# Optimization experiments

Hardware: AMD Instinct MI355X
Metric: run time of the kernel (lower is better)

The kernel has to match this reference:

```python
import jax, jax.numpy as jnp
import numpy as np

# Param packing order: [capacitance_x, capacitance_y] + for each direction in
# (ax, by, xy, yx, xx, yy): [conductance, mean, std, pot]  -> total 26 scalars.
_DIR = {"ax": 0, "by": 1, "xy": 2, "yx": 3, "xx": 4, "yy": 5}

B, T = 4096, 4096


def setup_inputs() -> dict:
    key = jax.random.key(0)
    inputs = jax.random.normal(key, (B, T, 2), dtype=jnp.float32)
    # initializer constants from the keras layer
    params = jnp.asarray([1.0, 1.0] + [0.001, 0.3, 3.0, 1.0] * 6, dtype=jnp.float32)
    return {"inputs": inputs, "params": params}


def reference(inputs, params):
    cap_x, cap_y = params[0], params[1]

    def syn(d, pre, post):
        i = 2 + 4 * _DIR[d]
        g, mean, std, pot = params[i], params[i + 1], params[i + 2], params[i + 3]
        return g * jax.nn.sigmoid(std * (pre - mean)) * (pot - post)

    def step(state, inp):
        x, y = state                      # each [B, 1]
        a, b = inp[:, :1], inp[:, 1:]     # each [B, 1]
        cur_x = syn("ax", a, x) + syn("yx", y, x) + syn("xx", x, x)
        cur_y = syn("by", b, y) + syn("xy", x, y) + syn("yy", y, y)
        x = x + cur_x / cap_x
        y = y + cur_y / cap_y
        out = jnp.concatenate((x, y), axis=-1)  # [B, 2]
        return (x, y), out

    bsz = inputs.shape[0]
    x0 = jnp.zeros((bsz, 1), inputs.dtype)
    y0 = jnp.ones((bsz, 1), inputs.dtype)   # initial state = concat(zeros, ones)
    _, outs = jax.lax.scan(step, (x0, y0), jnp.swapaxes(inputs, 0, 1))  # [T, B, 2]
    return jnp.swapaxes(outs, 0, 1)  # [B, T, 2]
```

## Files before the change

### kernel.cpp

```cpp
#include <hip/hip_runtime.h>

#define TLEN  4096
#define NROWS 4096
#define RPB   32
#define K     32
#define NC    (TLEN / K)
#define LDPAD 66
#define SGSL  (16 * 32)
#define STSL  (RPB * LDPAD)
#define UN    8

__device__ __forceinline__ float fexp2(float x) { return __builtin_amdgcn_exp2f(x); }
__device__ __forceinline__ float frcp(float x)  { return __builtin_amdgcn_rcpf(x); }
__device__ __forceinline__ float sigz(float z)  { return frcp(1.0f + fexp2(z)); }

__device__ __forceinline__ float lane_swap1(float v) {
    int r = __builtin_amdgcn_update_dpp(0, __float_as_int(v), 0xB1, 0xF, 0xF, true);
    return __int_as_float(r);
}

__device__ void run_fast(const float* __restrict__ inp, const float* __restrict__ prm,
                         float* __restrict__ out,
                         float4* __restrict__ sgbuf,
                         float*  __restrict__ st) {
    const int tid  = threadIdx.x;
    const int wid  = tid >> 6;
    const int lane = tid & 63;
    const int R0   = blockIdx.x * RPB;
    const float L2E = 1.4426950408889634f;
    float2* __restrict__ out2 = (float2*)out;

    if (wid == 1) {
        const int r = lane & 31, h = lane >> 5;
        const float c1x = -prm[4] * L2E, c0x = prm[4] * prm[3] * L2E;
        const float c1y = -prm[8] * L2E, c0y = prm[8] * prm[7] * L2E;
        const float4* __restrict__ src = (const float4*)inp + (size_t)(R0 + r) * (TLEN / 2);

        auto produce = [&](int c) {
            float4* sl = sgbuf + ((c & 1) ? SGSL : 0);
            const int base = c * 16 + h * 8;
#pragma unroll
            for (int j = 0; j < 8; ++j) {
                float4 v = src[base + j];
                float4 o;
                o.x = sigz(__builtin_fmaf(c1x, v.x, c0x));
                o.y = sigz(__builtin_fmaf(c1y, v.y, c0y));
                o.z = sigz(__builtin_fmaf(c1x, v.z, c0x));
                o.w = sigz(__builtin_fmaf(c1y, v.w, c0y));
                sl[(h * 8 + j) * 32 + r] = o;
            }
        };
        auto flush = [&](int c) {
            const float* sl = st + ((c & 1) ? STSL : 0);
            const int col = lane & 31;
#pragma unroll
            for (int j = 0; j < 16; ++j) {
                int ro = 2 * j + (lane >> 5);
                float2 v = *(const float2*)&sl[ro * LDPAD + col * 2];
                out2[(size_t)(R0 + ro) * TLEN + (size_t)c * K + col] = v;
            }
        };

        produce(0);
        __syncthreads();
        for (int c = 0; c < NC; ++c) {
            if (c + 1 < NC) produce(c + 1);
            if (c >= 1)     flush(c - 1);
            __syncthreads();
        }
        flush(NC - 1);
    } else {
        const int r_  = lane >> 1;
        const int par = lane & 1;
        const int inB = par ? 6 : 2, sfB = par ? 22 : 18, t2B = par ? 10 : 14;
        const float ic  = 1.0f / prm[par];
        const float g1  = prm[sfB] * ic, P1 = g1 * prm[sfB + 3], Gn1 = -g1;
        const float g2  = prm[t2B] * ic, P2 = g2 * prm[t2B + 3], Gn2 = -g2;
        const float gA  = prm[inB] * ic, PA = gA * prm[inB + 3], GnA = -gA;
        const float sdz = prm[sfB + 2];
        const float c1s = -sdz * L2E, c0s = sdz * prm[sfB + 1] * L2E;

        float x   = par ? 1.0f : 0.0f;
        float sig = sigz(__builtin_fmaf(c1s, x, c0s));
        float u   = __builtin_fmaf(-sig, sig, sig);
        float q   = 0.5f - sig;

        auto step = [&](float sg, float* wp, int t) {
            float Av  = __builtin_fmaf(GnA, x, PA);
            float t1v = __builtin_fmaf(Gn1, x, P1);
            float t2v = __builtin_fmaf(Gn2, x, P2);
            float m   = sg * Av;
            float b2  = __builtin_fmaf(sig, t1v, m);
            float sc  = lane_swap1(sig);
            float dx  = __builtin_fmaf(sc, t2v, b2);
            x = x + dx;
            wp[2 * t] = x;
            float dz = sdz * dx;
            float tt = __builtin_fmaf(q, dz, 1.0f);
            float aa = dz * tt;
            sig = __builtin_fmaf(u, aa, sig);
            u   = __builtin_fmaf(-sig, sig, sig);
            q   = 0.5f - sig;
        };

        __syncthreads();
        for (int c = 0; c < NC; ++c) {
            const float4* lb = sgbuf + ((c & 1) ? SGSL : 0);
            float* wp = st + ((c & 1) ? STSL : 0) + r_ * LDPAD + par;
            float4 f0 = lb[r_];
            float4 f1 = lb[32 + r_];
#pragma unroll
            for (int tp = 0; tp < 16; ++tp) {
                float4 f = f0; f0 = f1;
                if (tp < 14) f1 = lb[(tp + 2) * 32 + r_];
                step(par ? f.y : f.x, wp, 2 * tp);
                step(par ? f.w : f.z, wp, 2 * tp + 1);
            }
            sig = sigz(__builtin_fmaf(c1s, x, c0s));
            u   = __builtin_fmaf(-sig, sig, sig);
            q   = 0.5f - sig;
            __syncthreads();
        }
    }
}

struct LaneConst {
    float c1_in, c0_in, c1_sf, c0_sf, c1_ot, c0_ot;
    float gS_in, gS_cr, gS_sf, gP_in, gP_cr, gP_sf;
};

template<bool SHARED>
__device__ __forceinline__ float do_step_exact(float s, float pre_in, const LaneConst& k) {
    float sig_in = sigz(__builtin_fmaf(k.c1_in, pre_in, k.c0_in));
    float sig_sf = sigz(__builtin_fmaf(k.c1_sf, s, k.c0_sf));
    float sig_ot;
    if (SHARED) sig_ot = sig_sf;
    else        sig_ot = sigz(__builtin_fmaf(k.c1_ot, s, k.c0_ot));
    float sig_cr = lane_swap1(sig_ot);
    float S = __builtin_fmaf(k.gS_in, sig_in, __builtin_fmaf(k.gS_cr, sig_cr, k.gS_sf * sig_sf));
    float P = __builtin_fmaf(k.gP_in, sig_in, __builtin_fmaf(k.gP_cr, sig_cr, k.gP_sf * sig_sf));
    return s + __builtin_fmaf(S, -s, P);
}

template<bool SHARED>
__device__ void run_exact(const float* __restrict__ inp, const float* __restrict__ prm,
                          float* __restrict__ out) {
    const int tid = blockIdx.x * 128 + threadIdx.x;
    const int row = tid >> 1;
    if (row >= NROWS) return;
    const int par = tid & 1;
    const float L2E = 1.4426950408889634f;
    const int inB = par ? 6 : 2, sfB = par ? 22 : 18, otB = par ? 14 : 10, crB = par ? 10 : 14;
    const float invc = 1.0f / prm[par];
    LaneConst k;
    float sd = prm[inB + 2], mn = prm[inB + 1];
    k.c1_in = -sd * L2E; k.c0_in = sd * mn * L2E;
    sd = prm[sfB + 2]; mn = prm[sfB + 1];
    k.c1_sf = -sd * L2E; k.c0_sf = sd * mn * L2E;
    sd = prm[otB + 2]; mn = prm[otB + 1];
    k.c1_ot = -sd * L2E; k.c0_ot = sd * mn * L2E;
    k.gS_in = prm[inB] * invc; k.gP_in = k.gS_in * prm[inB + 3];
    k.gS_sf = prm[sfB] * invc; k.gP_sf = k.gS_sf * prm[sfB + 3];
    k.gS_cr = prm[crB] * invc; k.gP_cr = k.gS_cr * prm[crB + 3];

    const float4* __restrict__ src = (const float4*)inp + (size_t)row * (TLEN / 2);
    float* __restrict__ dst = out + (size_t)row * (TLEN * 2) + par;
    float s = par ? 1.0f : 0.0f;

    float4 cur[UN], nxt[UN];
#pragma unroll
    for (int j = 0; j < UN; ++j) cur[j] = src[j];
    const int NIT = TLEN / (2 * UN);
    for (int it = 0; it < NIT; ++it) {
        if (it + 1 < NIT) {
#pragma unroll
            for (int j = 0; j < UN; ++j) nxt[j] = src[(it + 1) * UN + j];
        }
        float* dptr = dst + it * (UN * 4);
#pragma unroll
        for (int j = 0; j < UN; ++j) {
            float4 f = cur[j];
            s = do_step_exact<SHARED>(s, par ? f.y : f.x, k);
            dptr[j * 4] = s;
            s = do_step_exact<SHARED>(s, par ? f.w : f.z, k);
            dptr[j * 4 + 2] = s;
        }
#pragma unroll
        for (int j = 0; j < UN; ++j) cur[j] = nxt[j];
    }
}

__global__ __launch_bounds__(128, 1)
void memcell_scan(const float* __restrict__ inp, const float* __restrict__ prm,
                  float* __restrict__ out) {
    __shared__ float4 sgbuf[2 * SGSL];
    __shared__ float  st[2 * STSL];

    const bool shared = (prm[11] == prm[19]) && (prm[12] == prm[20]) &&
                        (prm[15] == prm[23]) && (prm[16] == prm[24]);
    const float capx = prm[0], capy = prm[1];
    const bool gpos = prm[2] >= 0.f && prm[6] >= 0.f && prm[10] >= 0.f &&
                      prm[14] >= 0.f && prm[18] >= 0.f && prm[22] >= 0.f &&
                      capx > 0.f && capy > 0.f;
    const float sx = (prm[2] + prm[14] + prm[18]) / capx;
    const float sy = (prm[6] + prm[10] + prm[22]) / capy;
    const float lox = fminf(0.f, fminf(prm[5], fminf(prm[17], prm[21])));
    const float hix = fmaxf(0.f, fmaxf(prm[5], fmaxf(prm[17], prm[21])));
    const float loy = fminf(1.f, fminf(prm[9], fminf(prm[13], prm[25])));
    const float hiy = fmaxf(1.f, fmaxf(prm[9], fmaxf(prm[13], prm[25])));
    const float wbx = prm[20] * sx * (hix - lox), wby = prm[24] * sy * (hiy - loy);
    const float zmx = prm[20] * fmaxf(fabsf(lox - prm[19]), fabsf(hix - prm[19]));
    const float zmy = prm[24] * fmaxf(fabsf(loy - prm[23]), fabsf(hiy - prm[23]));
    const bool fast = shared && gpos && sx <= 0.25f && sy <= 0.25f &&
                      wbx <= 0.05f && wby <= 0.05f && zmx <= 20.f && zmy <= 20.f;
    if (fast) {
        run_fast(inp, prm, out, sgbuf, st);
    } else {
        if (shared) run_exact<true >(inp, prm, out);
        else        run_exact<false>(inp, prm, out);
    }
}

extern "C" void kernel_launch(void* const* d_in, const int* in_sizes, int n_in,
                              void* d_out, int out_size, void* d_ws, size_t ws_size,
                              hipStream_t stream) {
    (void)in_sizes; (void)n_in; (void)d_ws; (void)ws_size; (void)out_size;
    const float* inp = (const float*)d_in[0];
    const float* prm = (const float*)d_in[1];
    float* out = (float*)d_out;
    memcell_scan<<<dim3(NROWS / RPB), dim3(128), 0, stream>>>(inp, prm, out);
}
```

Baseline: 351.3 us.

## Precompute input-synapse coefficients in producer and compute exact sigmoid per step

The producer wave now folds the input-synapse conductance and potential into the staged values, so the consumer's input term becomes a single FMA per step. The consumer replaces the Taylor-style incremental sigmoid update with an exact exp2/rcp sigmoid on every step. This removes the parameter-range guard that selected the fast path. Shared-memory layouts are reworked so each lane (one row and one state variable) reads its own float4 and writes its own padded row. The change puts a transcendental back on the serial dependency chain in exchange for accuracy and a simpler input term, and it doubles the staged LDS footprint.

```diff
diff --git a/kernel.cpp b/kernel.cpp
--- a/kernel.cpp
+++ b/kernel.cpp
@@ -5,9 +5,9 @@
 #define RPB   32
 #define K     32
 #define NC    (TLEN / K)
-#define LDPAD 66
-#define SGSL  (16 * 32)
-#define STSL  (RPB * LDPAD)
+#define SGSL  (16 * 64)
+#define STP   33
+#define STSL  (64 * STP)
 #define UN    8
 
 __device__ __forceinline__ float fexp2(float x) { return __builtin_amdgcn_exp2f(x); }
@@ -34,20 +34,27 @@
         const int r = lane & 31, h = lane >> 5;
         const float c1x = -prm[4] * L2E, c0x = prm[4] * prm[3] * L2E;
         const float c1y = -prm[8] * L2E, c0y = prm[8] * prm[7] * L2E;
+        const float gAx = prm[2] / prm[0], PAx = gAx * prm[5], GnAx = -gAx;
+        const float gAy = prm[6] / prm[1], PAy = gAy * prm[9], GnAy = -gAy;
         const float4* __restrict__ src = (const float4*)inp + (size_t)(R0 + r) * (TLEN / 2);
 
         auto produce = [&](int c) {
             float4* sl = sgbuf + ((c & 1) ? SGSL : 0);
-            const int base = c * 16 + h * 8;
+            const int base = c * 16;
 #pragma unroll
             for (int j = 0; j < 8; ++j) {
-                float4 v = src[base + j];
-                float4 o;
-                o.x = sigz(__builtin_fmaf(c1x, v.x, c0x));
-                o.y = sigz(__builtin_fmaf(c1y, v.y, c0y));
-                o.z = sigz(__builtin_fmaf(c1x, v.z, c0x));
-                o.w = sigz(__builtin_fmaf(c1y, v.w, c0y));
-                sl[(h * 8 + j) * 32 + r] = o;
+                const int tp = h * 8 + j;
+                float4 v = src[base + tp];
+                float sx0 = sigz(__builtin_fmaf(c1x, v.x, c0x));
+                float sy0 = sigz(__builtin_fmaf(c1y, v.y, c0y));
+                float sx1 = sigz(__builtin_fmaf(c1x, v.z, c0x));
+                float sy1 = sigz(__builtin_fmaf(c1y, v.w, c0y));
+                float4 ox; ox.x = GnAx * sx0; ox.y = PAx * sx0;
+                           ox.z = GnAx * sx1; ox.w = PAx * sx1;
+                float4 oy; oy.x = GnAy * sy0; oy.y = PAy * sy0;
+                           oy.z = GnAy * sy1; oy.w = PAy * sy1;
+                sl[tp * 64 + 2 * r]     = ox;
+                sl[tp * 64 + 2 * r + 1] = oy;
             }
         };
         auto flush = [&](int c) {
@@ -56,7 +63,9 @@
 #pragma unroll
             for (int j = 0; j < 16; ++j) {
                 int ro = 2 * j + (lane >> 5);
-                float2 v = *(const float2*)&sl[ro * LDPAD + col * 2];
+                float2 v;
+                v.x = sl[(2 * ro)     * STP + col];
+                v.y = sl[(2 * ro + 1) * STP + col];
                 out2[(size_t)(R0 + ro) * TLEN + (size_t)c * K + col] = v;
             }
         };
@@ -70,55 +79,42 @@
         }
         flush(NC - 1);
     } else {
-        const int r_  = lane >> 1;
         const int par = lane & 1;
-        const int inB = par ? 6 : 2, sfB = par ? 22 : 18, t2B = par ? 10 : 14;
+        const int sfB = par ? 22 : 18, t2B = par ? 10 : 14;
         const float ic  = 1.0f / prm[par];
         const float g1  = prm[sfB] * ic, P1 = g1 * prm[sfB + 3], Gn1 = -g1;
         const float g2  = prm[t2B] * ic, P2 = g2 * prm[t2B + 3], Gn2 = -g2;
-        const float gA  = prm[inB] * ic, PA = gA * prm[inB + 3], GnA = -gA;
         const float sdz = prm[sfB + 2];
         const float c1s = -sdz * L2E, c0s = sdz * prm[sfB + 1] * L2E;
 
         float x   = par ? 1.0f : 0.0f;
         float sig = sigz(__builtin_fmaf(c1s, x, c0s));
-        float u   = __builtin_fmaf(-sig, sig, sig);
-        float q   = 0.5f - sig;
-
-        auto step = [&](float sg, float* wp, int t) {
-            float Av  = __builtin_fmaf(GnA, x, PA);
+
+        auto step = [&](float a, float b, float* wp, int t) {
+            float m   = __builtin_fmaf(a, x, b);
             float t1v = __builtin_fmaf(Gn1, x, P1);
             float t2v = __builtin_fmaf(Gn2, x, P2);
-            float m   = sg * Av;
             float b2  = __builtin_fmaf(sig, t1v, m);
             float sc  = lane_swap1(sig);
             float dx  = __builtin_fmaf(sc, t2v, b2);
             x = x + dx;
-            wp[2 * t] = x;
-            float dz = sdz * dx;
-            float tt = __builtin_fmaf(q, dz, 1.0f);
-            float aa = dz * tt;
-            sig = __builtin_fmaf(u, aa, sig);
-            u   = __builtin_fmaf(-sig, sig, sig);
-            q   = 0.5f - sig;
+            wp[t] = x;
+            sig = sigz(__builtin_fmaf(c1s, x, c0s));
         };
 
         __syncthreads();
         for (int c = 0; c < NC; ++c) {
             const float4* lb = sgbuf + ((c & 1) ? SGSL : 0);
-            float* wp = st + ((c & 1) ? STSL : 0) + r_ * LDPAD + par;
-            float4 f0 = lb[r_];
-            float4 f1 = lb[32 + r_];
+            float* wp = st + ((c & 1) ? STSL : 0) + lane * STP;
+            float4 f0 = lb[lane];
+            float4 f1 = lb[64 + lane];
 #pragma unroll
             for (int tp = 0; tp < 16; ++tp) {
                 float4 f = f0; f0 = f1;
-                if (tp < 14) f1 = lb[(tp + 2) * 32 + r_];
-                step(par ? f.y : f.x, wp, 2 * tp);
-                step(par ? f.w : f.z, wp, 2 * tp + 1);
+                if (tp < 14) f1 = lb[(tp + 2) * 64 + lane];
+                step(f.x, f.y, wp, 2 * tp);
+                step(f.z, f.w, wp, 2 * tp + 1);
             }
-            sig = sigz(__builtin_fmaf(c1s, x, c0s));
-            u   = __builtin_fmaf(-sig, sig, sig);
-            q   = 0.5f - sig;
             __syncthreads();
         }
     }
@@ -129,20 +125,16 @@
     float gS_in, gS_cr, gS_sf, gP_in, gP_cr, gP_sf;
 };
 
-template<bool SHARED>
 __device__ __forceinline__ float do_step_exact(float s, float pre_in, const LaneConst& k) {
     float sig_in = sigz(__builtin_fmaf(k.c1_in, pre_in, k.c0_in));
     float sig_sf = sigz(__builtin_fmaf(k.c1_sf, s, k.c0_sf));
-    float sig_ot;
-    if (SHARED) sig_ot = sig_sf;
-    else        sig_ot = sigz(__builtin_fmaf(k.c1_ot, s, k.c0_ot));
+    float sig_ot = sigz(__builtin_fmaf(k.c1_ot, s, k.c0_ot));
     float sig_cr = lane_swap1(sig_ot);
     float S = __builtin_fmaf(k.gS_in, sig_in, __builtin_fmaf(k.gS_cr, sig_cr, k.gS_sf * sig_sf));
     float P = __builtin_fmaf(k.gP_in, sig_in, __builtin_fmaf(k.gP_cr, sig_cr, k.gP_sf * sig_sf));
     return s + __builtin_fmaf(S, -s, P);
 }
 
-template<bool SHARED>
 __device__ void run_exact(const float* __restrict__ inp, const float* __restrict__ prm,
                           float* __restrict__ out) {
     const int tid = blockIdx.x * 128 + threadIdx.x;
@@ -180,9 +172,9 @@
 #pragma unroll
         for (int j = 0; j < UN; ++j) {
             float4 f = cur[j];
-            s = do_step_exact<SHARED>(s, par ? f.y : f.x, k);
+            s = do_step_exact(s, par ? f.y : f.x, k);
             dptr[j * 4] = s;
-            s = do_step_exact<SHARED>(s, par ? f.w : f.z, k);
+            s = do_step_exact(s, par ? f.w : f.z, k);
             dptr[j * 4 + 2] = s;
         }
 #pragma unroll
@@ -198,26 +190,10 @@
 
     const bool shared = (prm[11] == prm[19]) && (prm[12] == prm[20]) &&
                         (prm[15] == prm[23]) && (prm[16] == prm[24]);
-    const float capx = prm[0], capy = prm[1];
-    const bool gpos = prm[2] >= 0.f && prm[6] >= 0.f && prm[10] >= 0.f &&
-                      prm[14] >= 0.f && prm[18] >= 0.f && prm[22] >= 0.f &&
-                      capx > 0.f && capy > 0.f;
-    const float sx = (prm[2] + prm[14] + prm[18]) / capx;
-    const float sy = (prm[6] + prm[10] + prm[22]) / capy;
-    const float lox = fminf(0.f, fminf(prm[5], fminf(prm[17], prm[21])));
-    const float hix = fmaxf(0.f, fmaxf(prm[5], fmaxf(prm[17], prm[21])));
-    const float loy = fminf(1.f, fminf(prm[9], fminf(prm[13], prm[25])));
-    const float hiy = fmaxf(1.f, fmaxf(prm[9], fmaxf(prm[13], prm[25])));
-    const float wbx = prm[20] * sx * (hix - lox), wby = prm[24] * sy * (hiy - loy);
-    const float zmx = prm[20] * fmaxf(fabsf(lox - prm[19]), fabsf(hix - prm[19]));
-    const float zmy = prm[24] * fmaxf(fabsf(loy - prm[23]), fabsf(hiy - prm[23]));
-    const bool fast = shared && gpos && sx <= 0.25f && sy <= 0.25f &&
-                      wbx <= 0.05f && wby <= 0.05f && zmx <= 20.f && zmy <= 20.f;
-    if (fast) {
+    if (shared) {
         run_fast(inp, prm, out, sgbuf, st);
     } else {
-        if (shared) run_exact<true >(inp, prm, out);
-        else        run_exact<false>(inp, prm, out);
+        run_exact(inp, prm, out);
     }
 }
 
```

New measurement: 371.2 us. 1.06x slower.
